# Kernel optimization log

Hardware: AMD Instinct MI355X
Metric: run time of the kernel (lower is better)

The kernel has to match this reference:

```python
import jax, jax.numpy as jnp
import numpy as np

M = 8192      # nodes
D = 128       # feature dim
DEG = 32      # neighbors per node


def setup_inputs() -> dict:
    key = jax.random.key(0)
    ks = jax.random.split(key, 6)
    z = jax.random.normal(ks[0], (M, D), dtype=jnp.float32)
    # deterministic, duplicate-free edge list: node i -> (i+1..i+DEG) mod M
    src = jnp.repeat(jnp.arange(M, dtype=jnp.int64), DEG)
    dst = (src + jnp.tile(jnp.arange(1, DEG + 1, dtype=jnp.int64), M)) % M
    edge_index = jnp.stack([src, dst], axis=0)  # [2, M*DEG]
    s = 1.0 / np.sqrt(D)
    Wg = jax.random.normal(ks[1], (D, D), dtype=jnp.float32) * s
    Wc = jax.random.normal(ks[2], (D, D), dtype=jnp.float32) * s
    Wq = jax.random.normal(ks[3], (D, D), dtype=jnp.float32) * s
    Wk = jax.random.normal(ks[4], (D, D), dtype=jnp.float32) * s
    a = jax.random.normal(ks[5], (2 * D,), dtype=jnp.float32)
    return {"z": z, "edge_index": edge_index, "Wg": Wg, "Wc": Wc,
            "Wq": Wq, "Wk": Wk, "a": a}


def reference(z, edge_index, Wg, Wc, Wq, Wk, a):
    m, d = z.shape
    wg = z @ Wg.T                              # [m, d]
    src, dst = edge_index[0], edge_index[1]
    a_src, a_dst = a[:d], a[d:]
    # per-edge score: leaky_relu(a . [wg[i], wg[j]]) = leaky_relu(a1.wg[i] + a2.wg[j])
    scores = jax.nn.leaky_relu((wg @ a_src)[src] + (wg @ a_dst)[dst])  # [E]
    # softmax over each source node's neighbors (segment softmax)
    smax = jax.ops.segment_max(scores, src, num_segments=m)
    ex = jnp.exp(scores - smax[src])
    denom = jax.ops.segment_sum(ex, src, num_segments=m)
    alpha = ex / denom[src]                    # [E]
    # scatter-aggregate: local[i] = sum_j alpha_ij * wg[j]
    local = jax.ops.segment_sum(alpha[:, None] * wg[dst], src, num_segments=m)
    # dense global attention branch
    q = z @ Wq.T
    k = z @ Wk.T
    beta = jax.nn.softmax(q @ k.T / jnp.sqrt(jnp.float32(d)), axis=-1)  # [m, m]
    global_msg = beta @ (z @ Wc.T)
    return jax.nn.leaky_relu(local + global_msg + z)
```

## Files before the change

kernel.cpp:

```cpp
#include <hip/hip_runtime.h>

#define MM 8192
#define DD 128
#define DEG 32
#define KSPLIT 8

typedef __attribute__((ext_vector_type(8))) _Float16 h8;
typedef __attribute__((ext_vector_type(4))) float f4;
typedef __attribute__((ext_vector_type(4))) unsigned int u4;
typedef __attribute__((ext_vector_type(4))) short s4;

__device__ __forceinline__ unsigned short f2h(float f) {
  _Float16 h = (_Float16)f;
  return __builtin_bit_cast(unsigned short, h);
}

__device__ __forceinline__ void lds_dma16(const unsigned short* gptr, unsigned short* lptr) {
  __builtin_amdgcn_global_load_lds(
      (const __attribute__((address_space(1))) unsigned int*)gptr,
      (__attribute__((address_space(3))) unsigned int*)lptr, 16, 0, 0);
}

__global__ __launch_bounds__(256) void proj_kernel(
    const float* __restrict__ z, const float* __restrict__ Wg,
    const float* __restrict__ Wc, const float* __restrict__ Wq,
    const float* __restrict__ Wk, const float* __restrict__ a,
    float* __restrict__ wg, unsigned short* __restrict__ qb,
    unsigned short* __restrict__ kb, unsigned short* __restrict__ ct,
    float* __restrict__ sg, float* __restrict__ sd)
{
  __shared__ unsigned short zt[64 * 136];
  __shared__ unsigned short wt[128 * 136];
  const int mode = blockIdx.y;
  const float* __restrict__ W = (mode == 0) ? Wg : (mode == 1) ? Wq : (mode == 2) ? Wk : Wc;
  const int r0 = blockIdx.x * 64;
  const int tid = threadIdx.x;

  #pragma unroll
  for (int it = 0; it < 8; ++it) {
    int id = tid + it * 256, row = id >> 5, c4 = (id & 31) * 4;
    f4 v = *(const f4*)(z + (r0 + row) * DD + c4);
    s4 sv = {(short)f2h(v.x), (short)f2h(v.y), (short)f2h(v.z), (short)f2h(v.w)};
    *(s4*)&zt[row * 136 + c4] = sv;
  }
  #pragma unroll
  for (int it = 0; it < 16; ++it) {
    int id = tid + it * 256, row = id >> 5, c4 = (id & 31) * 4;
    f4 v = *(const f4*)(W + row * DD + c4);
    s4 sv = {(short)f2h(v.x), (short)f2h(v.y), (short)f2h(v.z), (short)f2h(v.w)};
    *(s4*)&wt[row * 136 + c4] = sv;
  }
  __syncthreads();

  const int lane = tid & 63, w = tid >> 6, n = lane & 15, quad = lane >> 4;
  h8 afr[4];
  #pragma unroll
  for (int kt = 0; kt < 4; ++kt)
    afr[kt] = *(const h8*)&zt[(16 * w + n) * 136 + kt * 32 + quad * 8];

  f4 acc[8];
  const f4 fzero = {0.f, 0.f, 0.f, 0.f};
  #pragma unroll
  for (int nt = 0; nt < 8; ++nt) {
    f4 c = fzero;
    #pragma unroll
    for (int kt = 0; kt < 4; ++kt) {
      h8 b = *(const h8*)&wt[(16 * nt + n) * 136 + kt * 32 + quad * 8];
      c = __builtin_amdgcn_mfma_f32_16x16x32_f16(afr[kt], b, c, 0, 0, 0);
    }
    acc[nt] = c;
  }

  if (mode == 0) {
    #pragma unroll
    for (int nt = 0; nt < 8; ++nt)
      #pragma unroll
      for (int r = 0; r < 4; ++r)
        wg[(r0 + 16 * w + quad * 4 + r) * DD + 16 * nt + n] = acc[nt][r];
    float av[8], bv[8];
    #pragma unroll
    for (int nt = 0; nt < 8; ++nt) { av[nt] = a[16 * nt + n]; bv[nt] = a[DD + 16 * nt + n]; }
    #pragma unroll
    for (int r = 0; r < 4; ++r) {
      float s1 = 0.f, s2 = 0.f;
      #pragma unroll
      for (int nt = 0; nt < 8; ++nt) { s1 += acc[nt][r] * av[nt]; s2 += acc[nt][r] * bv[nt]; }
      s1 += __shfl_xor(s1, 1); s1 += __shfl_xor(s1, 2); s1 += __shfl_xor(s1, 4); s1 += __shfl_xor(s1, 8);
      s2 += __shfl_xor(s2, 1); s2 += __shfl_xor(s2, 2); s2 += __shfl_xor(s2, 4); s2 += __shfl_xor(s2, 8);
      if (n == 0) {
        int g = r0 + 16 * w + quad * 4 + r;
        sg[g] = s1; sd[g] = s2;
      }
    }
  } else if (mode == 1) {
    const float qscale = 0.08838834764831845f;
    #pragma unroll
    for (int nt = 0; nt < 8; ++nt)
      #pragma unroll
      for (int r = 0; r < 4; ++r)
        qb[(r0 + 16 * w + quad * 4 + r) * DD + 16 * nt + n] = f2h(acc[nt][r] * qscale);
  } else if (mode == 2) {
    #pragma unroll
    for (int nt = 0; nt < 8; ++nt)
      #pragma unroll
      for (int r = 0; r < 4; ++r)
        kb[(r0 + 16 * w + quad * 4 + r) * DD + 16 * nt + n] = f2h(acc[nt][r]);
  } else {
    __syncthreads();
    #pragma unroll
    for (int nt = 0; nt < 8; ++nt)
      #pragma unroll
      for (int r = 0; r < 4; ++r)
        wt[(16 * nt + n) * 80 + 16 * w + quad * 4 + r] = f2h(acc[nt][r]);
    __syncthreads();
    #pragma unroll
    for (int it = 0; it < 4; ++it) {
      int idx = tid + it * 256, d = idx >> 3, c8 = (idx & 7) * 8;
      u4 v = *(const u4*)&wt[d * 80 + c8];
      *(u4*)(ct + (size_t)d * MM + r0 + c8) = v;
    }
  }
}

__global__ __launch_bounds__(128) void edge_kernel(
    const int* __restrict__ ei, const float* __restrict__ wg,
    const float* __restrict__ sg, const float* __restrict__ sd,
    float* __restrict__ loc)
{
  __shared__ float alpha_s[DEG];
  __shared__ int dst_s[DEG];
  const int i = blockIdx.x, tid = threadIdx.x;
  if (tid < DEG) {
    int dstj = ei[MM * DEG + i * DEG + tid];
    float s = sg[i] + sd[dstj];
    s = s > 0.f ? s : 0.01f * s;
    float mx = s;
    #pragma unroll
    for (int off = 1; off < DEG; off <<= 1) mx = fmaxf(mx, __shfl_xor(mx, off));
    float p = __expf(s - mx);
    float sum = p;
    #pragma unroll
    for (int off = 1; off < DEG; off <<= 1) sum += __shfl_xor(sum, off);
    alpha_s[tid] = p / sum;
    dst_s[tid] = dstj;
  }
  __syncthreads();
  float accum = 0.f;
  #pragma unroll 8
  for (int j = 0; j < DEG; ++j)
    accum += alpha_s[j] * wg[(size_t)dst_s[j] * DD + tid];
  loc[(size_t)i * DD + tid] = accum;
}

__global__ __launch_bounds__(256, 2) void flash_kernel(
    const unsigned short* __restrict__ qb, const unsigned short* __restrict__ kb,
    const unsigned short* __restrict__ ct, unsigned short* __restrict__ Opart,
    float* __restrict__ Lpart)
{
  __shared__ unsigned short sh[37376];
  const int bx = blockIdx.x, ck = blockIdx.y;
  const int tid = threadIdx.x, lane = tid & 63, w = tid >> 6;
  const int n = lane & 15, quad = lane >> 4;
  const int ln = n, lq = quad;
  const int qr0 = bx * 128;

  #pragma unroll
  for (int it = 0; it < 8; ++it)
    lds_dma16(qb + (qr0 + it * 16 + ln) * DD + w * 32 + lq * 8,
              &sh[(it * 256 + tid) * 8]);
  __syncthreads();
  h8 aq[2][4];
  #pragma unroll
  for (int mt = 0; mt < 2; ++mt)
    #pragma unroll
    for (int kt = 0; kt < 4; ++kt)
      aq[mt][kt] = *(const h8*)&sh[((w * 2 + mt) * 4 + kt) * 512 + lane * 8];
  __syncthreads();

  const unsigned short* kp = kb + (size_t)(ck * 1024 + 4 * ln) * DD + w * 32 + lq * 8;
  const unsigned short* vp = ct + (size_t)(16 * (w >> 1) + ln) * MM + ck * 1024 + (w & 1) * 32 + lq * 8;

  #pragma unroll
  for (int it = 0; it < 4; ++it)
    lds_dma16(kp + it * DD, &sh[(it * 256 + tid) * 8]);
  #pragma unroll
  for (int it = 0; it < 4; ++it)
    lds_dma16(vp + (size_t)it * 32 * MM, &sh[8192 + (it * 256 + tid) * 8]);

  f4 acc_o[2][8];
  const f4 fzero = {0.f, 0.f, 0.f, 0.f};
  #pragma unroll
  for (int mt = 0; mt < 2; ++mt)
    #pragma unroll
    for (int dt = 0; dt < 8; ++dt) acc_o[mt][dt] = fzero;
  float l_r[2][4] = {{0.f, 0.f, 0.f, 0.f}, {0.f, 0.f, 0.f, 0.f}};
  const int pbase = 32768 + w * 1152;

  for (int t = 0; t < 16; ++t) {
    __syncthreads();
    const int cur = (t & 1) * 16384;

    if (t < 15) {
      const int nb = ((t + 1) & 1) * 16384;
      const unsigned short* kpn = kp + (size_t)(t + 1) * 64 * DD;
      const unsigned short* vpn = vp + (t + 1) * 64;
      #pragma unroll
      for (int it = 0; it < 4; ++it)
        lds_dma16(kpn + it * DD, &sh[nb + (it * 256 + tid) * 8]);
      #pragma unroll
      for (int it = 0; it < 4; ++it)
        lds_dma16(vpn + (size_t)it * 32 * MM, &sh[nb + 8192 + (it * 256 + tid) * 8]);
    }

    f4 accs[2][4];
    #pragma unroll
    for (int mt = 0; mt < 2; ++mt)
      #pragma unroll
      for (int nt = 0; nt < 4; ++nt) accs[mt][nt] = fzero;
    #pragma unroll
    for (int nt = 0; nt < 4; ++nt) {
      #pragma unroll
      for (int kt = 0; kt < 4; ++kt) {
        h8 bk = *(const h8*)&sh[cur + nt * 2048 + kt * 512 + lane * 8];
        accs[0][nt] = __builtin_amdgcn_mfma_f32_16x16x32_f16(aq[0][kt], bk, accs[0][nt], 0, 0, 0);
        accs[1][nt] = __builtin_amdgcn_mfma_f32_16x16x32_f16(aq[1][kt], bk, accs[1][nt], 0, 0, 0);
      }
    }

    h8 ap[2][2];
    #pragma unroll
    for (int mt = 0; mt < 2; ++mt) {
      #pragma unroll
      for (int r = 0; r < 4; ++r) {
        float p0 = __expf(fminf(accs[mt][0][r], 10.f));
        float p1 = __expf(fminf(accs[mt][1][r], 10.f));
        float p2 = __expf(fminf(accs[mt][2][r], 10.f));
        float p3 = __expf(fminf(accs[mt][3][r], 10.f));
        l_r[mt][r] += p0 + p1 + p2 + p3;
        unsigned int lo = ((unsigned int)f2h(p1) << 16) | f2h(p0);
        unsigned int hi = ((unsigned int)f2h(p3) << 16) | f2h(p2);
        uint2 pv; pv.x = lo; pv.y = hi;
        *(uint2*)&sh[pbase + (quad * 4 + r) * 72 + n * 4] = pv;
      }
      ap[mt][0] = *(const h8*)&sh[pbase + n * 72 + quad * 8];
      ap[mt][1] = *(const h8*)&sh[pbase + n * 72 + 32 + quad * 8];
    }

    #pragma unroll
    for (int dt = 0; dt < 8; ++dt) {
      #pragma unroll
      for (int k2 = 0; k2 < 2; ++k2) {
        h8 bv = *(const h8*)&sh[cur + 8192 + dt * 1024 + k2 * 512 + lane * 8];
        acc_o[0][dt] = __builtin_amdgcn_mfma_f32_16x16x32_f16(ap[0][k2], bv, acc_o[0][dt], 0, 0, 0);
        acc_o[1][dt] = __builtin_amdgcn_mfma_f32_16x16x32_f16(ap[1][k2], bv, acc_o[1][dt], 0, 0, 0);
      }
    }
  }

  #pragma unroll
  for (int mt = 0; mt < 2; ++mt)
    #pragma unroll
    for (int r = 0; r < 4; ++r) {
      float lv = l_r[mt][r];
      lv += __shfl_xor(lv, 1); lv += __shfl_xor(lv, 2);
      lv += __shfl_xor(lv, 4); lv += __shfl_xor(lv, 8);
      int g = qr0 + w * 32 + mt * 16 + quad * 4 + r;
      if (n == 0) Lpart[ck * MM + g] = lv;
      #pragma unroll
      for (int dt = 0; dt < 8; ++dt)
        Opart[((size_t)ck * MM + g) * DD + 16 * dt + n] = f2h(acc_o[mt][dt][r]);
    }
}

__global__ __launch_bounds__(256) void merge_kernel(
    const unsigned short* __restrict__ Opart, const float* __restrict__ Lpart,
    const float* __restrict__ loc, const float* __restrict__ z,
    float* __restrict__ out)
{
  int gid = blockIdx.x * 256 + threadIdx.x;
  int g = gid >> 4, c8 = (gid & 15) * 8;
  float l = 0.f;
  float o[8] = {0.f, 0.f, 0.f, 0.f, 0.f, 0.f, 0.f, 0.f};
  #pragma unroll
  for (int ck = 0; ck < KSPLIT; ++ck) {
    l += Lpart[ck * MM + g];
    h8 v = *(const h8*)(Opart + ((size_t)ck * MM + g) * DD + c8);
    #pragma unroll
    for (int j = 0; j < 8; ++j) o[j] += (float)v[j];
  }
  float inv = 1.0f / l;
  const float* lp = loc + (size_t)g * DD + c8;
  const float* zp = z + (size_t)g * DD + c8;
  float* op = out + (size_t)g * DD + c8;
  #pragma unroll
  for (int j = 0; j < 8; ++j) {
    float r = o[j] * inv + lp[j] + zp[j];
    op[j] = r > 0.f ? r : 0.01f * r;
  }
}

extern "C" void kernel_launch(void* const* d_in, const int* in_sizes, int n_in,
                              void* d_out, int out_size, void* d_ws, size_t ws_size,
                              hipStream_t stream) {
  const float* z  = (const float*)d_in[0];
  const int*   ei = (const int*)d_in[1];
  const float* Wg = (const float*)d_in[2];
  const float* Wc = (const float*)d_in[3];
  const float* Wq = (const float*)d_in[4];
  const float* Wk = (const float*)d_in[5];
  const float* a  = (const float*)d_in[6];
  float* out = (float*)d_out;
  char* ws = (char*)d_ws;

  float*          wg    = (float*)(ws + 0);
  unsigned short* qb    = (unsigned short*)(ws + (4 << 20));
  unsigned short* kb    = (unsigned short*)(ws + (6 << 20));
  unsigned short* ct    = (unsigned short*)(ws + (8 << 20));
  float*          sg    = (float*)(ws + (10 << 20));
  float*          sd    = (float*)(ws + (10 << 20) + (64 << 10));
  float*          loc   = (float*)(ws + (11 << 20));
  unsigned short* Opart = (unsigned short*)(ws + (15 << 20));
  float*          Lpart = (float*)(ws + (31 << 20));

  proj_kernel<<<dim3(128, 4), 256, 0, stream>>>(z, Wg, Wc, Wq, Wk, a, wg, qb, kb, ct, sg, sd);
  edge_kernel<<<8192, 128, 0, stream>>>(ei, wg, sg, sd, loc);
  flash_kernel<<<dim3(64, KSPLIT), 256, 0, stream>>>(qb, kb, ct, Opart, Lpart);
  merge_kernel<<<512, 256, 0, stream>>>(Opart, Lpart, loc, z, out);
}
```

Measured before the change: 135.8 us.

## Fuse edge softmax aggregation into merge kernel with LDS-staged neighbor rows

Removes the separate edge_kernel and computes the segment softmax and neighbor aggregation inside merge_kernel, for 16 nodes per block. This drops one launch and the round trip of the loc buffer through global memory. The block stages a 48-row window of wg into LDS, because neighbors of consecutive nodes overlap. Neighbors outside that window are read from global memory instead. The cost is more work per merge block and a serial softmax done by 16 threads.

New measurement: 126.0 us. 7.2% less time.

```diff
diff --git a/kernel.cpp b/kernel.cpp
--- a/kernel.cpp
+++ b/kernel.cpp
@@ -4,6 +4,8 @@
 #define DD 128
 #define DEG 32
 #define KSPLIT 8
+#define NB 16
+#define RSTAGE 48
 
 typedef __attribute__((ext_vector_type(8))) _Float16 h8;
 typedef __attribute__((ext_vector_type(4))) float f4;
@@ -122,36 +124,6 @@
   }
 }
 
-__global__ __launch_bounds__(128) void edge_kernel(
-    const int* __restrict__ ei, const float* __restrict__ wg,
-    const float* __restrict__ sg, const float* __restrict__ sd,
-    float* __restrict__ loc)
-{
-  __shared__ float alpha_s[DEG];
-  __shared__ int dst_s[DEG];
-  const int i = blockIdx.x, tid = threadIdx.x;
-  if (tid < DEG) {
-    int dstj = ei[MM * DEG + i * DEG + tid];
-    float s = sg[i] + sd[dstj];
-    s = s > 0.f ? s : 0.01f * s;
-    float mx = s;
-    #pragma unroll
-    for (int off = 1; off < DEG; off <<= 1) mx = fmaxf(mx, __shfl_xor(mx, off));
-    float p = __expf(s - mx);
-    float sum = p;
-    #pragma unroll
-    for (int off = 1; off < DEG; off <<= 1) sum += __shfl_xor(sum, off);
-    alpha_s[tid] = p / sum;
-    dst_s[tid] = dstj;
-  }
-  __syncthreads();
-  float accum = 0.f;
-  #pragma unroll 8
-  for (int j = 0; j < DEG; ++j)
-    accum += alpha_s[j] * wg[(size_t)dst_s[j] * DD + tid];
-  loc[(size_t)i * DD + tid] = accum;
-}
-
 __global__ __launch_bounds__(256, 2) void flash_kernel(
     const unsigned short* __restrict__ qb, const unsigned short* __restrict__ kb,
     const unsigned short* __restrict__ ct, unsigned short* __restrict__ Opart,
@@ -273,29 +245,84 @@
 }
 
 __global__ __launch_bounds__(256) void merge_kernel(
+    const int* __restrict__ ei, const float* __restrict__ wg,
+    const float* __restrict__ sg, const float* __restrict__ sd,
     const unsigned short* __restrict__ Opart, const float* __restrict__ Lpart,
-    const float* __restrict__ loc, const float* __restrict__ z,
-    float* __restrict__ out)
+    const float* __restrict__ z, float* __restrict__ out)
 {
-  int gid = blockIdx.x * 256 + threadIdx.x;
-  int g = gid >> 4, c8 = (gid & 15) * 8;
+  __shared__ float rows_s[RSTAGE * 132];
+  __shared__ float sc_s[NB][DEG];
+  __shared__ float alpha_s[NB][DEG];
+  __shared__ int idx_s[NB][DEG];
+  const int tid = threadIdx.x;
+  const int i0 = blockIdx.x * NB;
+
+  #pragma unroll
+  for (int it = 0; it < 6; ++it) {
+    int idx = tid + it * 256;
+    int r = idx >> 5, c4 = (idx & 31) * 4;
+    int grow = (i0 + 1 + r) & (MM - 1);
+    *(f4*)&rows_s[r * 132 + c4] = *(const f4*)(wg + (size_t)grow * DD + c4);
+  }
+  #pragma unroll
+  for (int it = 0; it < 2; ++it) {
+    int e = tid + it * 256;
+    int ni = e >> 5, j = e & 31;
+    int i = i0 + ni;
+    int dstj = ei[MM * DEG + i * DEG + j];
+    float s = sg[i] + sd[dstj];
+    sc_s[ni][j] = s > 0.f ? s : 0.01f * s;
+    idx_s[ni][j] = (dstj - (i0 + 1)) & (MM - 1);
+  }
+  __syncthreads();
+
+  if (tid < NB) {
+    float mx = -1e30f;
+    #pragma unroll 8
+    for (int j = 0; j < DEG; ++j) mx = fmaxf(mx, sc_s[tid][j]);
+    float sum = 0.f;
+    #pragma unroll 8
+    for (int j = 0; j < DEG; ++j) { float p = __expf(sc_s[tid][j] - mx); alpha_s[tid][j] = p; sum += p; }
+    float inv = 1.f / sum;
+    #pragma unroll 8
+    for (int j = 0; j < DEG; ++j) alpha_s[tid][j] *= inv;
+  }
+  __syncthreads();
+
+  const int ni = tid >> 4, d0 = (tid & 15) * 8;
+  const int i = i0 + ni;
+  float acc[8] = {0.f, 0.f, 0.f, 0.f, 0.f, 0.f, 0.f, 0.f};
+  #pragma unroll 4
+  for (int j = 0; j < DEG; ++j) {
+    float al = alpha_s[ni][j];
+    int r = idx_s[ni][j];
+    if (r < RSTAGE) {
+      const float* src = &rows_s[r * 132 + d0];
+      #pragma unroll
+      for (int q = 0; q < 8; ++q) acc[q] += al * src[q];
+    } else {
+      const float* src = wg + (size_t)((i0 + 1 + r) & (MM - 1)) * DD + d0;
+      #pragma unroll
+      for (int q = 0; q < 8; ++q) acc[q] += al * src[q];
+    }
+  }
+
   float l = 0.f;
   float o[8] = {0.f, 0.f, 0.f, 0.f, 0.f, 0.f, 0.f, 0.f};
   #pragma unroll
   for (int ck = 0; ck < KSPLIT; ++ck) {
-    l += Lpart[ck * MM + g];
-    h8 v = *(const h8*)(Opart + ((size_t)ck * MM + g) * DD + c8);
-    #pragma unroll
-    for (int j = 0; j < 8; ++j) o[j] += (float)v[j];
+    l += Lpart[ck * MM + i];
+    h8 v = *(const h8*)(Opart + ((size_t)ck * MM + i) * DD + d0);
+    #pragma unroll
+    for (int q = 0; q < 8; ++q) o[q] += (float)v[q];
   }
   float inv = 1.0f / l;
-  const float* lp = loc + (size_t)g * DD + c8;
-  const float* zp = z + (size_t)g * DD + c8;
-  float* op = out + (size_t)g * DD + c8;
-  #pragma unroll
-  for (int j = 0; j < 8; ++j) {
-    float r = o[j] * inv + lp[j] + zp[j];
-    op[j] = r > 0.f ? r : 0.01f * r;
+  const float* zp = z + (size_t)i * DD + d0;
+  float* op = out + (size_t)i * DD + d0;
+  #pragma unroll
+  for (int q = 0; q < 8; ++q) {
+    float r = o[q] * inv + acc[q] + zp[q];
+    op[q] = r > 0.f ? r : 0.01f * r;
   }
 }
 
@@ -318,12 +345,10 @@
   unsigned short* ct    = (unsigned short*)(ws + (8 << 20));
   float*          sg    = (float*)(ws + (10 << 20));
   float*          sd    = (float*)(ws + (10 << 20) + (64 << 10));
-  float*          loc   = (float*)(ws + (11 << 20));
   unsigned short* Opart = (unsigned short*)(ws + (15 << 20));
   float*          Lpart = (float*)(ws + (31 << 20));
 
   proj_kernel<<<dim3(128, 4), 256, 0, stream>>>(z, Wg, Wc, Wq, Wk, a, wg, qb, kb, ct, sg, sd);
-  edge_kernel<<<8192, 128, 0, stream>>>(ei, wg, sg, sd, loc);
   flash_kernel<<<dim3(64, KSPLIT), 256, 0, stream>>>(qb, kb, ct, Opart, Lpart);
-  merge_kernel<<<512, 256, 0, stream>>>(Opart, Lpart, loc, z, out);
-}
+  merge_kernel<<<512, 256, 0, stream>>>(ei, wg, sg, sd, Opart, Lpart, z, out);
+}
```
